# Kernel optimization log

Measured on AMD Instinct MI355X. Metric: run time of the kernel, lower is better.

## Reference

```python
import jax, jax.numpy as jnp
import numpy as np

B = 256
C_IN, F_IN = 32, 256
C_OUT, F_OUT = 32, 256
KERNEL_SIZE = 4
BN_EPS = 1e-5


def _block_mask():
    # channel-wise connectivity: output channel o sees input channels in its kernel_size block
    co = jnp.arange(C_OUT)[:, None] // KERNEL_SIZE
    ci = jnp.arange(C_IN)[None, :] // KERNEL_SIZE
    return co == ci  # [C_OUT, C_IN] bool


def setup_inputs() -> dict:
    key = jax.random.key(0)
    k_x, k_w, k_b, k_g, k_be = jax.random.split(key, 5)
    x = jax.random.normal(k_x, (B, C_IN, F_IN), dtype=jnp.float32)
    fan_in = KERNEL_SIZE * F_IN
    W = jax.random.normal(k_w, (C_OUT, C_IN, F_OUT, F_IN), dtype=jnp.float32) / np.float32(np.sqrt(fan_in))
    bias = jax.random.normal(k_b, (C_OUT, F_OUT), dtype=jnp.float32) * 0.01
    gamma = 1.0 + 0.1 * jax.random.normal(k_g, (C_OUT * F_OUT,), dtype=jnp.float32)
    beta = 0.1 * jax.random.normal(k_be, (C_OUT * F_OUT,), dtype=jnp.float32)
    mask = _block_mask()
    return {"x": x, "W": W, "bias": bias, "gamma": gamma, "beta": beta, "mask": mask}


def reference(x, W, bias, gamma, beta, mask):
    # masked sparse linear: y[b,o,f] = sum_{c,i} mask[o,c] * W[o,c,f,i] * x[b,c,i] + bias[o,f]
    Wm = W * mask[:, :, None, None].astype(W.dtype)
    y = jnp.einsum('bci,ocfi->bof', x, Wm) + bias  # [B, C_OUT, F_OUT]
    b = y.shape[0]
    yf = y.reshape(b, C_OUT * F_OUT)
    # BatchNorm1d in training mode: biased batch statistics over the batch dim
    mean = jnp.mean(yf, axis=0)
    var = jnp.var(yf, axis=0)
    yn = (yf - mean) * jax.lax.rsqrt(var + BN_EPS) * gamma + beta
    # Swish: x * sigmoid(x)
    out = yn * jax.nn.sigmoid(yn)
    return out.reshape(b, C_OUT, F_OUT)
```

## Files before the change

kernel.cpp:

```cpp
#include <hip/hip_runtime.h>
#include <hip/hip_bf16.h>


typedef float  f32x4  __attribute__((ext_vector_type(4)));
typedef short  short8 __attribute__((ext_vector_type(8)));
typedef unsigned short u16x8 __attribute__((ext_vector_type(8)));

static __device__ __forceinline__ unsigned short f2bf(float f) {
    unsigned int u = __float_as_uint(f);
    u += 0x7FFFu + ((u >> 16) & 1u);
    return (unsigned short)(u >> 16);
}

#define GLL(gp, lp) __builtin_amdgcn_global_load_lds( \
    (const __attribute__((address_space(1))) unsigned int*)(gp), \
    (__attribute__((address_space(3))) unsigned int*)(lp), 16, 0, 0)

__global__ __launch_bounds__(256) void conv_kernel(const float* __restrict__ x,
                                                   unsigned short* __restrict__ xb) {
    const int base = blockIdx.x * 1024 + threadIdx.x;
#pragma unroll
    for (int i = 0; i < 4; ++i) {
        const int cid = base + i * 256;
        const f32x4 a = *(const f32x4*)(x + (size_t)cid * 8);
        const f32x4 b = *(const f32x4*)(x + (size_t)cid * 8 + 4);
        u16x8 v;
        v[0] = f2bf(a[0]); v[1] = f2bf(a[1]); v[2] = f2bf(a[2]); v[3] = f2bf(a[3]);
        v[4] = f2bf(b[0]); v[5] = f2bf(b[1]); v[6] = f2bf(b[2]); v[7] = f2bf(b[3]);
        *(u16x8*)(xb + (size_t)cid * 8) = v;
    }
}

__global__ __launch_bounds__(256, 2) void fused_kernel(
    const unsigned short* __restrict__ xb, const float* __restrict__ W,
    const float* __restrict__ gamma, const float* __restrict__ beta,
    float* __restrict__ out)
{
    __shared__ __align__(16) char ldsA[2][32768];
    __shared__ __align__(16) char ldsB[2][4096];
    __shared__ float wps1[4][32], wps2[4][32];
    __shared__ float sa[32], sb[32];

    const int bid = blockIdx.x;
    const int g   = bid & 7;
    const int nt  = bid >> 3;
    const int o   = g * 4 + (nt >> 3);
    const int f0  = (nt & 7) * 32;
    const int gcol0 = o * 256 + f0;

    const int t    = threadIdx.x;
    const int wave = t >> 6;
    const int lane = t & 63;
    const int lr   = lane & 15;
    const int kq   = lane >> 4;

    f32x4 acc[4][2];
    const f32x4 zero = {0.f, 0.f, 0.f, 0.f};
#pragma unroll
    for (int i = 0; i < 4; ++i) { acc[i][0] = zero; acc[i][1] = zero; }

    f32x4 breg[4][2];

    auto ISSUE_W = [&](int st) {
        const int cp = st >> 2, kc = (st & 3) * 64;
        const float* bsrc = W + ((size_t)((o * 32 + g * 4 + cp) * 256 + f0)) * 256 + kc
                              + (size_t)(t >> 3) * 256 + (t & 7) * 8;
        breg[st & 3][0] = *(const f32x4*)bsrc;
        breg[st & 3][1] = *(const f32x4*)(bsrc + 4);
    };
    auto ISSUE_A = [&](int st) {
        const unsigned short* asrc = xb + g * 1024 + st * 64;
        char* Ab = ldsA[st & 1];
#pragma unroll
        for (int i = 0; i < 8; ++i) {
            const int cid = i * 256 + t;
            const int r = cid >> 3, c = cid & 7;
            GLL(asrc + (size_t)r * 8192 + (c ^ (r & 7)) * 8, Ab + cid * 16);
        }
    };
    auto WRITEB = [&](int st) {
        const int n = t >> 3, c = t & 7;
        short8 v;
        v[0] = (short)f2bf(breg[st & 3][0][0]); v[1] = (short)f2bf(breg[st & 3][0][1]);
        v[2] = (short)f2bf(breg[st & 3][0][2]); v[3] = (short)f2bf(breg[st & 3][0][3]);
        v[4] = (short)f2bf(breg[st & 3][1][0]); v[5] = (short)f2bf(breg[st & 3][1][1]);
        v[6] = (short)f2bf(breg[st & 3][1][2]); v[7] = (short)f2bf(breg[st & 3][1][3]);
        *(short8*)(ldsB[st & 1] + n * 128 + ((c ^ (n & 7)) * 16)) = v;
    };
    auto COMPUTE = [&](int st) {
        const char* Ab = ldsA[st & 1];
        const char* Bb = ldsB[st & 1];
#pragma unroll
        for (int ks = 0; ks < 2; ++ks) {
            short8 af[4], bfr[2];
#pragma unroll
            for (int i = 0; i < 4; ++i) {
                const int ra = wave * 64 + i * 16 + lr;
                af[i] = *(const short8*)(Ab + ra * 128 + (((ks * 4 + kq) ^ (ra & 7)) * 16));
            }
#pragma unroll
            for (int j = 0; j < 2; ++j) {
                const int n = j * 16 + lr;
                bfr[j] = *(const short8*)(Bb + n * 128 + (((ks * 4 + kq) ^ (n & 7)) * 16));
            }
#pragma unroll
            for (int i = 0; i < 4; ++i)
#pragma unroll
                for (int j = 0; j < 2; ++j)
                    acc[i][j] = __builtin_amdgcn_mfma_f32_16x16x32_bf16(af[i], bfr[j], acc[i][j], 0, 0, 0);
        }
    };

    ISSUE_W(0);
    ISSUE_A(0);
    ISSUE_W(1);
    ISSUE_W(2);
    ISSUE_W(3);
    WRITEB(0);
    asm volatile("s_waitcnt vmcnt(6)" ::: "memory");
    asm volatile("s_waitcnt lgkmcnt(0)" ::: "memory");
    __builtin_amdgcn_s_barrier();

#pragma unroll
    for (int st = 0; st < 16; ++st) {
        COMPUTE(st);
        if (st < 15) {
            ISSUE_A(st + 1);
            if (st < 12) ISSUE_W(st + 4);
            WRITEB(st + 1);
            if (st < 12) {
                asm volatile("s_waitcnt vmcnt(2)" ::: "memory");
            } else {
                asm volatile("s_waitcnt vmcnt(0)" ::: "memory");
            }
            asm volatile("s_waitcnt lgkmcnt(0)" ::: "memory");
            __builtin_amdgcn_s_barrier();
        }
    }

    float s1[2] = {0.f, 0.f}, s2[2] = {0.f, 0.f};
#pragma unroll
    for (int i = 0; i < 4; ++i)
#pragma unroll
        for (int j = 0; j < 2; ++j)
#pragma unroll
            for (int r = 0; r < 4; ++r) {
                const float v = acc[i][j][r];
                s1[j] += v; s2[j] += v * v;
            }
#pragma unroll
    for (int j = 0; j < 2; ++j) {
        s1[j] += __shfl_xor(s1[j], 16); s2[j] += __shfl_xor(s2[j], 16);
        s1[j] += __shfl_xor(s1[j], 32); s2[j] += __shfl_xor(s2[j], 32);
    }
    if (kq == 0) {
#pragma unroll
        for (int j = 0; j < 2; ++j) {
            wps1[wave][j * 16 + lr] = s1[j];
            wps2[wave][j * 16 + lr] = s2[j];
        }
    }
    __syncthreads();
    if (t < 32) {
        float a1 = wps1[0][t] + wps1[1][t] + wps1[2][t] + wps1[3][t];
        float a2 = wps2[0][t] + wps2[1][t] + wps2[2][t] + wps2[3][t];
        const float mean = a1 * (1.0f / 256.0f);
        const float var  = a2 * (1.0f / 256.0f) - mean * mean;
        const float istd = rsqrtf(var + 1e-5f);
        const float ga = gamma[gcol0 + t];
        sa[t] = ga * istd;
        sb[t] = beta[gcol0 + t] - mean * ga * istd;
    }
    __syncthreads();

#pragma unroll
    for (int i = 0; i < 4; ++i) {
        const int row0 = wave * 64 + i * 16 + kq * 4;
#pragma unroll
        for (int j = 0; j < 2; ++j) {
            const int col = j * 16 + lr;
            const float a = sa[col], b2 = sb[col];
#pragma unroll
            for (int r = 0; r < 4; ++r) {
                const float z = a * acc[i][j][r] + b2;
                out[(size_t)(row0 + r) * 8192 + gcol0 + col] = z / (1.0f + expf(-z));
            }
        }
    }
}

extern "C" void kernel_launch(void* const* d_in, const int* in_sizes, int n_in,
                              void* d_out, int out_size, void* d_ws, size_t ws_size,
                              hipStream_t stream) {
    const float* x     = (const float*)d_in[0];
    const float* W     = (const float*)d_in[1];
    const float* gamma = (const float*)d_in[3];
    const float* beta  = (const float*)d_in[4];
    float* out = (float*)d_out;

    unsigned short* xb = (unsigned short*)d_ws;

    conv_kernel<<<256, 256, 0, stream>>>(x, xb);
    fused_kernel<<<256, 256, 0, stream>>>(xb, W, gamma, beta, out);
}
```

Before: 28.93 us.

## Fuse x bf16 conversion into main kernel via register-staged loads

Removes the separate kernel that converted x to bf16 and instead loads fp32 x tiles into registers, converts them in-kernel and writes them swizzled into LDS. The async global_load_lds path and the explicit vmcnt waits are replaced by compiler-managed register prefetch, with W prefetch depth cut from four stages to three. Rounding changes to a cheaper add-and-permute packing instead of round-to-nearest-even. This removes one launch and the xb round trip, but each block now rereads fp32 x and holds 16 extra vector registers, with launch bounds dropped to one block per SM.

```diff
diff --git a/kernel.cpp b/kernel.cpp
--- a/kernel.cpp
+++ b/kernel.cpp
@@ -4,35 +4,17 @@
 
 typedef float  f32x4  __attribute__((ext_vector_type(4)));
 typedef short  short8 __attribute__((ext_vector_type(8)));
-typedef unsigned short u16x8 __attribute__((ext_vector_type(8)));
+typedef unsigned int u32x2 __attribute__((ext_vector_type(2)));
+typedef unsigned int u32x4 __attribute__((ext_vector_type(4)));
 
-static __device__ __forceinline__ unsigned short f2bf(float f) {
-    unsigned int u = __float_as_uint(f);
-    u += 0x7FFFu + ((u >> 16) & 1u);
-    return (unsigned short)(u >> 16);
+static __device__ __forceinline__ unsigned int pkbf(float a, float b) {
+    const unsigned int u0 = __float_as_uint(a) + 0x8000u;
+    const unsigned int u1 = __float_as_uint(b) + 0x8000u;
+    return __builtin_amdgcn_perm(u1, u0, 0x07060302u);
 }
 
-#define GLL(gp, lp) __builtin_amdgcn_global_load_lds( \
-    (const __attribute__((address_space(1))) unsigned int*)(gp), \
-    (__attribute__((address_space(3))) unsigned int*)(lp), 16, 0, 0)
-
-__global__ __launch_bounds__(256) void conv_kernel(const float* __restrict__ x,
-                                                   unsigned short* __restrict__ xb) {
-    const int base = blockIdx.x * 1024 + threadIdx.x;
-#pragma unroll
-    for (int i = 0; i < 4; ++i) {
-        const int cid = base + i * 256;
-        const f32x4 a = *(const f32x4*)(x + (size_t)cid * 8);
-        const f32x4 b = *(const f32x4*)(x + (size_t)cid * 8 + 4);
-        u16x8 v;
-        v[0] = f2bf(a[0]); v[1] = f2bf(a[1]); v[2] = f2bf(a[2]); v[3] = f2bf(a[3]);
-        v[4] = f2bf(b[0]); v[5] = f2bf(b[1]); v[6] = f2bf(b[2]); v[7] = f2bf(b[3]);
-        *(u16x8*)(xb + (size_t)cid * 8) = v;
-    }
-}
-
-__global__ __launch_bounds__(256, 2) void fused_kernel(
-    const unsigned short* __restrict__ xb, const float* __restrict__ W,
+__global__ __launch_bounds__(256, 1) void fused_kernel(
+    const float* __restrict__ x, const float* __restrict__ W,
     const float* __restrict__ gamma, const float* __restrict__ beta,
     float* __restrict__ out)
 {
@@ -59,8 +41,31 @@
 #pragma unroll
     for (int i = 0; i < 4; ++i) { acc[i][0] = zero; acc[i][1] = zero; }
 
+    f32x4 areg[16];
     f32x4 breg[4][2];
 
+    auto A_LOAD = [&](int st) {
+        const float* asrc = x + g * 1024 + st * 64;
+#pragma unroll
+        for (int i = 0; i < 16; ++i) {
+            const int cid = i * 256 + t;
+            const int r = cid >> 4, c = cid & 15;
+            areg[i] = *(const f32x4*)(asrc + (size_t)r * 8192 + c * 4);
+        }
+    };
+    auto A_WRITE = [&](int st) {
+        char* Ab = ldsA[st & 1];
+#pragma unroll
+        for (int i = 0; i < 16; ++i) {
+            const int cid = i * 256 + t;
+            const int r = cid >> 4, c = cid & 15;
+            u32x2 d;
+            d[0] = pkbf(areg[i][0], areg[i][1]);
+            d[1] = pkbf(areg[i][2], areg[i][3]);
+            const int ch = c >> 1, half = c & 1;
+            *(u32x2*)(Ab + r * 128 + ((ch ^ (r & 7)) * 16) + half * 8) = d;
+        }
+    };
     auto ISSUE_W = [&](int st) {
         const int cp = st >> 2, kc = (st & 3) * 64;
         const float* bsrc = W + ((size_t)((o * 32 + g * 4 + cp) * 256 + f0)) * 256 + kc
@@ -68,24 +73,14 @@
         breg[st & 3][0] = *(const f32x4*)bsrc;
         breg[st & 3][1] = *(const f32x4*)(bsrc + 4);
     };
-    auto ISSUE_A = [&](int st) {
-        const unsigned short* asrc = xb + g * 1024 + st * 64;
-        char* Ab = ldsA[st & 1];
-#pragma unroll
-        for (int i = 0; i < 8; ++i) {
-            const int cid = i * 256 + t;
-            const int r = cid >> 3, c = cid & 7;
-            GLL(asrc + (size_t)r * 8192 + (c ^ (r & 7)) * 8, Ab + cid * 16);
-        }
-    };
     auto WRITEB = [&](int st) {
         const int n = t >> 3, c = t & 7;
-        short8 v;
-        v[0] = (short)f2bf(breg[st & 3][0][0]); v[1] = (short)f2bf(breg[st & 3][0][1]);
-        v[2] = (short)f2bf(breg[st & 3][0][2]); v[3] = (short)f2bf(breg[st & 3][0][3]);
-        v[4] = (short)f2bf(breg[st & 3][1][0]); v[5] = (short)f2bf(breg[st & 3][1][1]);
-        v[6] = (short)f2bf(breg[st & 3][1][2]); v[7] = (short)f2bf(breg[st & 3][1][3]);
-        *(short8*)(ldsB[st & 1] + n * 128 + ((c ^ (n & 7)) * 16)) = v;
+        u32x4 d;
+        d[0] = pkbf(breg[st & 3][0][0], breg[st & 3][0][1]);
+        d[1] = pkbf(breg[st & 3][0][2], breg[st & 3][0][3]);
+        d[2] = pkbf(breg[st & 3][1][0], breg[st & 3][1][1]);
+        d[3] = pkbf(breg[st & 3][1][2], breg[st & 3][1][3]);
+        *(u32x4*)(ldsB[st & 1] + n * 128 + ((c ^ (n & 7)) * 16)) = d;
     };
     auto COMPUTE = [&](int st) {
         const char* Ab = ldsA[st & 1];
@@ -111,28 +106,23 @@
         }
     };
 
+    A_LOAD(0);
     ISSUE_W(0);
-    ISSUE_A(0);
     ISSUE_W(1);
     ISSUE_W(2);
-    ISSUE_W(3);
+    A_WRITE(0);
     WRITEB(0);
-    asm volatile("s_waitcnt vmcnt(6)" ::: "memory");
     asm volatile("s_waitcnt lgkmcnt(0)" ::: "memory");
     __builtin_amdgcn_s_barrier();
 
 #pragma unroll
     for (int st = 0; st < 16; ++st) {
+        if (st < 15)  A_LOAD(st + 1);
+        if (st <= 12) ISSUE_W(st + 3);
         COMPUTE(st);
         if (st < 15) {
-            ISSUE_A(st + 1);
-            if (st < 12) ISSUE_W(st + 4);
+            A_WRITE(st + 1);
             WRITEB(st + 1);
-            if (st < 12) {
-                asm volatile("s_waitcnt vmcnt(2)" ::: "memory");
-            } else {
-                asm volatile("s_waitcnt vmcnt(0)" ::: "memory");
-            }
             asm volatile("s_waitcnt lgkmcnt(0)" ::: "memory");
             __builtin_amdgcn_s_barrier();
         }
@@ -198,8 +188,5 @@
     const float* beta  = (const float*)d_in[4];
     float* out = (float*)d_out;
 
-    unsigned short* xb = (unsigned short*)d_ws;
-
-    conv_kernel<<<256, 256, 0, stream>>>(x, xb);
-    fused_kernel<<<256, 256, 0, stream>>>(xb, W, gamma, beta, out);
+    fused_kernel<<<256, 256, 0, stream>>>(x, W, gamma, beta, out);
 }
```

Result: slower. 31.97 us (+10.5%).
